# Optimization experiments

Hardware: AMD Instinct MI355X
Metric: run time of the kernel (lower is better)

The kernel has to match this reference:

```python
import jax, jax.numpy as jnp
import numpy as np

D_MODEL = 32
N_HEADS = 4
D_K = 8
D_V = 8
LN_EPS = 1e-5
MASK_FILL = -1.0e9


def _layernorm(x, eps=LN_EPS):
    # torch.nn.LayerNorm with default affine params (gamma=1, beta=0)
    mu = jnp.mean(x, axis=-1, keepdims=True)
    var = jnp.var(x, axis=-1, keepdims=True)  # biased, matches torch
    return (x - mu) * jax.lax.rsqrt(var + eps)


def setup_inputs() -> dict:
    key = jax.random.key(0)
    ks = jax.random.split(key, 12)
    B, S = 8, 2048
    w = 1.0 / np.float32(np.sqrt(D_MODEL))
    return {
        "input_Q": jax.random.normal(ks[0], (B, S, D_MODEL), dtype=jnp.float32),
        "input_K": jax.random.normal(ks[1], (B, S, D_MODEL), dtype=jnp.float32),
        "input_V": jax.random.normal(ks[2], (B, S, D_MODEL), dtype=jnp.float32),
        "attn_mask": jax.random.randint(ks[3], (B, S, S), 0, 2).astype(jnp.bool_),
        "W_Q": jax.random.normal(ks[4], (D_MODEL, D_K * N_HEADS), dtype=jnp.float32) * w,
        "b_Q": jax.random.normal(ks[5], (D_K * N_HEADS,), dtype=jnp.float32) * 0.02,
        "W_K": jax.random.normal(ks[6], (D_MODEL, D_K * N_HEADS), dtype=jnp.float32) * w,
        "b_K": jax.random.normal(ks[7], (D_K * N_HEADS,), dtype=jnp.float32) * 0.02,
        "W_V": jax.random.normal(ks[8], (D_MODEL, D_V * N_HEADS), dtype=jnp.float32) * w,
        "b_V": jax.random.normal(ks[9], (D_V * N_HEADS,), dtype=jnp.float32) * 0.02,
        "W_O": jax.random.normal(ks[10], (D_V * N_HEADS, D_MODEL), dtype=jnp.float32) * w,
        "b_O": jax.random.normal(ks[11], (D_MODEL,), dtype=jnp.float32) * 0.02,
    }


def reference(input_Q, input_K, input_V, attn_mask, W_Q, b_Q, W_K, b_K, W_V, b_V, W_O, b_O):
    B, S, _ = input_Q.shape
    residual = input_Q
    # projections -> [B, H, S, d_head]
    Q = (input_Q @ W_Q + b_Q).reshape(B, S, N_HEADS, D_K).transpose(0, 2, 1, 3)
    K = (input_K @ W_K + b_K).reshape(B, S, N_HEADS, D_K).transpose(0, 2, 1, 3)
    V = (input_V @ W_V + b_V).reshape(B, S, N_HEADS, D_V).transpose(0, 2, 1, 3)
    scale = 1.0 / jnp.sqrt(jnp.asarray(D_K, dtype=Q.dtype))
    scores = jnp.einsum("bhqd,bhkd->bhqk", Q, K) * scale  # [B,H,S,S]
    scores = jnp.where(attn_mask[:, None, :, :], jnp.asarray(MASK_FILL, scores.dtype), scores)
    attn_ratio = jax.nn.softmax(scores, axis=-1)
    ctx = jnp.einsum("bhqk,bhkd->bhqd", attn_ratio, V)  # [B,H,S,Dv]
    self_attn = ctx.transpose(0, 2, 1, 3).reshape(B, S, N_HEADS * D_V)
    attn_output = self_attn @ W_O + b_O
    return (_layernorm(attn_output + residual), self_attn)
```

## Files before the change

### kernel.cpp

```cpp
#include <hip/hip_runtime.h>
#include <math.h>

#define D_MODEL 32
#define S_LEN   2048
#define B_SZ    8
#define NTOK    (B_SZ * S_LEN)
#define LN_EPS  1e-5f
#define LOG2E   1.44269504088896340736f
#define QK_SCALE 0.35355339059327373f
#define PROJ_BLKS (NTOK / 8)

typedef __attribute__((ext_vector_type(8)))  short    short8b;
typedef __attribute__((ext_vector_type(4)))  short    short4b;
typedef __attribute__((ext_vector_type(4)))  unsigned uint4v;
typedef __attribute__((ext_vector_type(16))) float    f32x16;

__device__ __forceinline__ unsigned short f2bf(float f) {
    unsigned u = __builtin_bit_cast(unsigned, f);
    unsigned r = (u + 0x7FFFu + ((u >> 16) & 1u)) >> 16;
    return (unsigned short)r;
}
__device__ __forceinline__ float bf2f(unsigned short h) {
    return __builtin_bit_cast(float, (unsigned)h << 16);
}
__device__ __forceinline__ unsigned cvtpk_bf16(float lo, float hi) {
    unsigned r;
    asm("v_cvt_pk_bf16_f32 %0, %1, %2" : "=v"(r) : "v"(lo), "v"(hi));
    return r;
}


__global__ __launch_bounds__(256) void prep_kernel(
    const void* __restrict__ mask,
    const float* __restrict__ xQ, const float* __restrict__ xK,
    const float* __restrict__ xV,
    const float* __restrict__ WQ, const float* __restrict__ bQ,
    const float* __restrict__ WK, const float* __restrict__ bK,
    const float* __restrict__ WV, const float* __restrict__ bV,
    unsigned short* __restrict__ QHC, unsigned short* __restrict__ QLC,
    unsigned short* __restrict__ KC,  unsigned short* __restrict__ VC,
    unsigned long long* __restrict__ pack)
{
    int bid = blockIdx.x;
    int t   = threadIdx.x;

    if (bid < 3 * PROJ_BLKS) {
        int which = bid / PROJ_BLKS;
        int xb    = bid - which * PROJ_BLKS;
        const float* x; const float* W; const float* bias; float scale;
        if (which == 0)      { x = xQ; W = WQ; bias = bQ; scale = QK_SCALE * LOG2E; }
        else if (which == 1) { x = xK; W = WK; bias = bK; scale = 1.0f; }
        else                 { x = xV; W = WV; bias = bV; scale = 1.0f; }

        __shared__ float xs[8][32];
        __shared__ float Ws[32][32];
        long base = (long)xb * 256;
        xs[t >> 5][t & 31] = x[base + t];
#pragma unroll
        for (int i = 0; i < 4; ++i) {
            int f = i * 256 + t;
            Ws[f >> 5][f & 31] = W[f];
        }
        __syncthreads();
        int r = t >> 5, j = t & 31;
        float acc = bias[j];
#pragma unroll
        for (int i = 0; i < 32; ++i) acc = fmaf(xs[r][i], Ws[i][j], acc);
        acc *= scale;

        long tok = (long)xb * 8 + r;
        long b   = tok >> 11;
        long ti  = tok & (S_LEN - 1);
        int  ch  = (int)(ti >> 5), kq = (int)(ti & 31);
        int  h   = j >> 3, d = j & 7;

        if (which == 0) {
            size_t qi = ((((size_t)b * 64 + ch) * 4 + h) * 32 + kq) * 8 + d;
            unsigned short hv = f2bf(acc);
            QHC[qi] = hv;
            QLC[qi] = f2bf(acc - bf2f(hv));
        } else if (which == 1) {
            size_t ki = (((((size_t)b * 64 + ch) * 4 + h) * 2 + 0) * 32 + kq) * 8 + d;
            unsigned short hv = f2bf(acc);
            KC[ki]       = hv;
            KC[ki + 256] = f2bf(acc - bf2f(hv));
        } else {
            size_t vi = (((size_t)b * 64 + ch) * 4 + h) * 256 + (size_t)d * 32 + kq;
            VC[vi] = f2bf(acc);
        }
    } else {
        int mb   = bid - 3 * PROJ_BLKS;
        long row = (long)mb * 4 + (t >> 6);
        int lane = t & 63;

        int probe = ((const int*)mask)[lane];
        bool is32 = (__ballot((probe & ~0xFF) == 0) == ~0ULL);

        unsigned long long* prow = pack + row * (S_LEN / 64);
        if (is32) {
            const int4* mr4 = (const int4*)((const int*)mask + row * S_LEN);
#pragma unroll
            for (int g = 0; g < 8; ++g) {
                int4 v = mr4[g * 64 + lane];
                unsigned long long b0 = __ballot(v.x != 0);
                unsigned long long b1 = __ballot(v.y != 0);
                unsigned long long b2 = __ballot(v.z != 0);
                unsigned long long b3 = __ballot(v.w != 0);
                if (lane == 0) {
                    prow[g * 4 + 0] = b0; prow[g * 4 + 1] = b1;
                    prow[g * 4 + 2] = b2; prow[g * 4 + 3] = b3;
                }
            }
        } else {
            const int* mri = (const int*)((const unsigned char*)mask + row * S_LEN);
#pragma unroll
            for (int g = 0; g < 8; ++g) {
                int v = mri[g * 64 + lane];
                unsigned long long b0 = __ballot((v & 0x000000FF) != 0);
                unsigned long long b1 = __ballot((v & 0x0000FF00) != 0);
                unsigned long long b2 = __ballot((v & 0x00FF0000) != 0);
                unsigned long long b3 = __ballot((v & 0xFF000000u) != 0);
                if (lane == 0) {
                    prow[g * 4 + 0] = b0; prow[g * 4 + 1] = b1;
                    prow[g * 4 + 2] = b2; prow[g * 4 + 3] = b3;
                }
            }
        }
    }
}

template<int NSEG>
__global__ __launch_bounds__(256, 4) void attn_kernel(
    const unsigned short* __restrict__ QHC, const unsigned short* __restrict__ QLC,
    const unsigned short* __restrict__ KC,  const unsigned short* __restrict__ VC,
    const unsigned long long* __restrict__ pack,
    float* __restrict__ pl, float* __restrict__ pctx)
{
    constexpr int SEGLEN = S_LEN / NSEG;
    constexpr int NGROUP = SEGLEN / 256;
    constexpr int NPT    = SEGLEN / 64;
    const int nb    = NSEG * 64;
    int raw   = blockIdx.x;
    int total = B_SZ * nb;
    int cpx   = total >> 3;
    int cid   = (raw & 7) * cpx + (raw >> 3);
    int b     = cid / nb;
    int rem   = cid - b * nb;
    int seg   = rem >> 6;
    int qt    = rem & 63;
    int h     = threadIdx.x >> 6;
    int lane  = threadIdx.x & 63;
    int q     = lane & 31;
    int half  = lane >> 5;
    int tok0  = qt * 32;
    long tokq = (long)b * S_LEN + tok0 + q;
    int k0    = seg * SEGLEN;
    int ch0   = k0 >> 5;

    f32x16 zero16;
#pragma unroll
    for (int i = 0; i < 16; ++i) zero16[i] = 0.0f;

    const unsigned long long* prow = pack + tokq * (S_LEN / 64);

    short ovv = (q == 8) ? (short)0x3F80 : (short)0;
    short8b ovf;
#pragma unroll
    for (int i = 0; i < 8; ++i) ovf[i] = ovv;

    size_t qoff = ((((size_t)b * 64 + qt) * 4 + h) * 32 + q) * 8;
    short8b qhf = *(const short8b*)(QHC + qoff);
    short8b qlf = *(const short8b*)(QLC + qoff);
    f32x16 cpv = zero16;

    const unsigned short* Kb0 = KC + (((size_t)b * 64) * 4 + h) * 512
                                   + (size_t)half * 256 + (size_t)q * 8;
    const unsigned short* Vb0 = VC + (((size_t)b * 64) * 4 + h) * 256
                                   + (size_t)q * 32 + half * 4;

    short8b kfA = *(const short8b*)(Kb0 + (size_t)ch0 * 2048);
    short8b kfB = *(const short8b*)(Kb0 + (size_t)(ch0 + 1) * 2048);
    short8b vf1c, vf2c;
    if (q < 8) {
        const unsigned short* vr = Vb0 + (size_t)ch0 * 1024;
        short4b a0 = *(const short4b*)(vr);
        short4b a1 = *(const short4b*)(vr + 8);
        short4b a2 = *(const short4b*)(vr + 16);
        short4b a3 = *(const short4b*)(vr + 24);
        vf1c = __builtin_shufflevector(a0, a1, 0, 1, 2, 3, 4, 5, 6, 7);
        vf2c = __builtin_shufflevector(a2, a3, 0, 1, 2, 3, 4, 5, 6, 7);
    } else { vf1c = ovf; vf2c = ovf; }

#pragma unroll
    for (int g = 0; g < NGROUP; ++g) {
        unsigned long long mg[4];
        mg[0] = prow[(k0 >> 6) + g * 4 + 0];
        mg[1] = prow[(k0 >> 6) + g * 4 + 1];
        mg[2] = prow[(k0 >> 6) + g * 4 + 2];
        mg[3] = prow[(k0 >> 6) + g * 4 + 3];

#pragma unroll 1
        for (int p = 0; p < 4; ++p) {
            int pa  = g * 4 + p;
            int chA = ch0 + 2 * pa;
            int chB = chA + 1;

            short8b kfA_n = kfA, kfB_n = kfB;
            if (pa + 1 < NPT) {
                kfA_n = *(const short8b*)(Kb0 + (size_t)(chA + 2) * 2048);
                kfB_n = *(const short8b*)(Kb0 + (size_t)(chB + 2) * 2048);
            }

            unsigned shA = (unsigned)(p * 16 + half);
            unsigned nA[4], nB[4];
#pragma unroll
            for (int c = 0; c < 4; ++c) {
                nA[c] = (unsigned)(mg[c] >> shA);
                nB[c] = (unsigned)(mg[c] >> (shA + 8u));
            }

            __builtin_amdgcn_s_setprio(1);
            f32x16 accA = __builtin_amdgcn_mfma_f32_32x32x16_bf16(kfA, qhf, zero16, 0, 0, 0);
            f32x16 accB = __builtin_amdgcn_mfma_f32_32x32x16_bf16(kfB, qhf, zero16, 0, 0, 0);
            accA = __builtin_amdgcn_mfma_f32_32x32x16_bf16(kfA, qlf, accA, 0, 0, 0);
            accB = __builtin_amdgcn_mfma_f32_32x32x16_bf16(kfB, qlf, accB, 0, 0, 0);
            __builtin_amdgcn_s_setprio(0);

            short8b vf1n, vf2n;
            if (q < 8) {
                const unsigned short* vr = Vb0 + (size_t)chB * 1024;
                short4b a0 = *(const short4b*)(vr);
                short4b a1 = *(const short4b*)(vr + 8);
                short4b a2 = *(const short4b*)(vr + 16);
                short4b a3 = *(const short4b*)(vr + 24);
                vf1n = __builtin_shufflevector(a0, a1, 0, 1, 2, 3, 4, 5, 6, 7);
                vf2n = __builtin_shufflevector(a2, a3, 0, 1, 2, 3, 4, 5, 6, 7);
            } else { vf1n = ovf; vf2n = ovf; }

            {
                unsigned pr[8];
#pragma unroll
                for (int j = 0; j < 8; ++j) {
                    const int c0 = (2 * j) & 3, c1 = (2 * j + 1) & 3;
                    const int s  = 2 * (j >> 1);
                    float p0 = ((nA[c0] >> s) & 1u) ? 0.0f
                             : __builtin_amdgcn_exp2f(accA[2 * j]);
                    float p1 = ((nA[c1] >> s) & 1u) ? 0.0f
                             : __builtin_amdgcn_exp2f(accA[2 * j + 1]);
                    pr[j] = cvtpk_bf16(p0, p1);
                }
                uint4v t1, t2;
                t1.x = pr[0]; t1.y = pr[1]; t1.z = pr[2]; t1.w = pr[3];
                t2.x = pr[4]; t2.y = pr[5]; t2.z = pr[6]; t2.w = pr[7];
                short8b pfa = __builtin_bit_cast(short8b, t1);
                short8b pfb = __builtin_bit_cast(short8b, t2);

                __builtin_amdgcn_s_setprio(1);
                cpv = __builtin_amdgcn_mfma_f32_32x32x16_bf16(vf1c, pfa, cpv, 0, 0, 0);
                cpv = __builtin_amdgcn_mfma_f32_32x32x16_bf16(vf2c, pfb, cpv, 0, 0, 0);
                __builtin_amdgcn_s_setprio(0);
            }

            short8b vf1nn, vf2nn;
            if (pa + 1 < NPT && q < 8) {
                const unsigned short* vr = Vb0 + (size_t)(chA + 2) * 1024;
                short4b a0 = *(const short4b*)(vr);
                short4b a1 = *(const short4b*)(vr + 8);
                short4b a2 = *(const short4b*)(vr + 16);
                short4b a3 = *(const short4b*)(vr + 24);
                vf1nn = __builtin_shufflevector(a0, a1, 0, 1, 2, 3, 4, 5, 6, 7);
                vf2nn = __builtin_shufflevector(a2, a3, 0, 1, 2, 3, 4, 5, 6, 7);
            } else { vf1nn = ovf; vf2nn = ovf; }

            {
                unsigned pr[8];
#pragma unroll
                for (int j = 0; j < 8; ++j) {
                    const int c0 = (2 * j) & 3, c1 = (2 * j + 1) & 3;
                    const int s  = 2 * (j >> 1);
                    float p0 = ((nB[c0] >> s) & 1u) ? 0.0f
                             : __builtin_amdgcn_exp2f(accB[2 * j]);
                    float p1 = ((nB[c1] >> s) & 1u) ? 0.0f
                             : __builtin_amdgcn_exp2f(accB[2 * j + 1]);
                    pr[j] = cvtpk_bf16(p0, p1);
                }
                uint4v t1, t2;
                t1.x = pr[0]; t1.y = pr[1]; t1.z = pr[2]; t1.w = pr[3];
                t2.x = pr[4]; t2.y = pr[5]; t2.z = pr[6]; t2.w = pr[7];
                short8b pfa = __builtin_bit_cast(short8b, t1);
                short8b pfb = __builtin_bit_cast(short8b, t2);

                __builtin_amdgcn_s_setprio(1);
                cpv = __builtin_amdgcn_mfma_f32_32x32x16_bf16(vf1n, pfa, cpv, 0, 0, 0);
                cpv = __builtin_amdgcn_mfma_f32_32x32x16_bf16(vf2n, pfb, cpv, 0, 0, 0);
                __builtin_amdgcn_s_setprio(0);
            }

            kfA = kfA_n;
            kfB = kfB_n;
            vf1c = vf1nn;
            vf2c = vf2nn;
        }
    }

    float4 cv = make_float4(cpv[0], cpv[1], cpv[2], cpv[3]);
    *(float4*)(pctx + ((size_t)seg * NTOK + tokq) * 32 + h * 8 + half * 4) = cv;
    if (half == 0)
        pl[(size_t)seg * NTOK * 4 + tokq * 4 + h] = cpv[4];
}

template<int NSEG>
__global__ __launch_bounds__(256) void combine_epilogue(
    const float* __restrict__ pl, const float* __restrict__ pctx,
    const float* __restrict__ WO, const float* __restrict__ bO,
    const float* __restrict__ resid,
    float* __restrict__ sa_out, float* __restrict__ out0)
{
    __shared__ float sas[8][32];
    __shared__ float Ws[32][32];
    int t = threadIdx.x;
    long base = (long)blockIdx.x * 256;
    int r = t >> 5, j = t & 31;
    long tok = (long)blockIdx.x * 8 + r;
    int h = j >> 3;

#pragma unroll
    for (int i = 0; i < 4; ++i) {
        int f = i * 256 + t;
        Ws[f >> 5][f & 31] = WO[f];
    }

    float L = 0.f, ctx = 0.f;
#pragma unroll
    for (int s2 = 0; s2 < NSEG; ++s2) {
        L   += pl[(size_t)s2 * NTOK * 4 + tok * 4 + h];
        ctx += pctx[((size_t)s2 * NTOK + tok) * 32 + j];
    }
    float sa = ctx / L;
    sa_out[base + t] = sa;
    sas[r][j] = sa;
    __syncthreads();

    float y = bO[j] + resid[base + t];
#pragma unroll
    for (int i = 0; i < 32; ++i) y = fmaf(sas[r][i], Ws[i][j], y);

    float sum = y;
#pragma unroll
    for (int o = 16; o >= 1; o >>= 1) sum += __shfl_xor(sum, o, 32);
    float mu = sum * (1.0f / 32.0f);
    float d  = y - mu;
    float sq = d * d;
#pragma unroll
    for (int o = 16; o >= 1; o >>= 1) sq += __shfl_xor(sq, o, 32);
    float var = sq * (1.0f / 32.0f);
    out0[base + t] = d * rsqrtf(var + LN_EPS);
}

extern "C" void kernel_launch(void* const* d_in, const int* in_sizes, int n_in,
                              void* d_out, int out_size, void* d_ws, size_t ws_size,
                              hipStream_t stream)
{
    const float* inQ = (const float*)d_in[0];
    const float* inK = (const float*)d_in[1];
    const float* inV = (const float*)d_in[2];
    const void*  mask = d_in[3];
    const float* WQ = (const float*)d_in[4];
    const float* bQ = (const float*)d_in[5];
    const float* WK = (const float*)d_in[6];
    const float* bK = (const float*)d_in[7];
    const float* WV = (const float*)d_in[8];
    const float* bV = (const float*)d_in[9];
    const float* WO = (const float*)d_in[10];
    const float* bO = (const float*)d_in[11];

    float* out0 = (float*)d_out;
    float* sa   = (float*)d_out + (long)NTOK * 32;

    char* ws = (char*)d_ws;
    unsigned short* QHC = (unsigned short*)(ws + 256);
    unsigned short* QLC = QHC + (size_t)NTOK * 32;
    unsigned short* KC  = QLC + (size_t)NTOK * 32;
    unsigned short* VC  = KC  + (size_t)NTOK * 64;
    unsigned long long* pack = (unsigned long long*)(VC + (size_t)NTOK * 32);
    float* pbase = (float*)(pack + (size_t)NTOK * (S_LEN / 64));

    size_t fixed  = 256 + 5ul * NTOK * 32 * 2 + (size_t)NTOK * (S_LEN / 64) * 8;
    size_t perseg = (size_t)NTOK * 36 * 4;
    int NS = 1;
    if (fixed + 2 * perseg <= ws_size) NS = 2;

    float* pl   = pbase;
    float* pctx = pl + (long)NS * NTOK * 4;

    prep_kernel<<<3 * PROJ_BLKS + NTOK / 4, 256, 0, stream>>>(
        mask, inQ, inK, inV, WQ, bQ, WK, bK, WV, bV, QHC, QLC, KC, VC, pack);

    int cgrid = NTOK / 8;
    switch (NS) {
    case 2: {
        int agrid = B_SZ * 2 * 64;
        attn_kernel<2><<<agrid, 256, 0, stream>>>(QHC, QLC, KC, VC, pack, pl, pctx);
        combine_epilogue<2><<<cgrid, 256, 0, stream>>>(pl, pctx, WO, bO, inQ, sa, out0);
        break;
    }
    default: {
        int agrid = B_SZ * 1 * 64;
        attn_kernel<1><<<agrid, 256, 0, stream>>>(QHC, QLC, KC, VC, pack, pl, pctx);
        combine_epilogue<1><<<cgrid, 256, 0, stream>>>(pl, pctx, WO, bO, inQ, sa, out0);
        break;
    }
    }
}
```

Before: 69.65 us.

## Fuse split-K attention segments and epilogue into one 512-thread block

```diff
diff --git a/kernel.cpp b/kernel.cpp
--- a/kernel.cpp
+++ b/kernel.cpp
@@ -129,33 +129,44 @@
     }
 }
 
-template<int NSEG>
-__global__ __launch_bounds__(256, 4) void attn_kernel(
+__global__ __launch_bounds__(512, 4) void attn_fused_kernel(
     const unsigned short* __restrict__ QHC, const unsigned short* __restrict__ QLC,
     const unsigned short* __restrict__ KC,  const unsigned short* __restrict__ VC,
     const unsigned long long* __restrict__ pack,
-    float* __restrict__ pl, float* __restrict__ pctx)
+    const float* __restrict__ WO, const float* __restrict__ bO,
+    const float* __restrict__ resid,
+    float* __restrict__ sa_out, float* __restrict__ out0)
 {
-    constexpr int SEGLEN = S_LEN / NSEG;
+    constexpr int SEGLEN = 1024;
     constexpr int NGROUP = SEGLEN / 256;
     constexpr int NPT    = SEGLEN / 64;
-    const int nb    = NSEG * 64;
-    int raw   = blockIdx.x;
-    int total = B_SZ * nb;
-    int cpx   = total >> 3;
-    int cid   = (raw & 7) * cpx + (raw >> 3);
-    int b     = cid / nb;
-    int rem   = cid - b * nb;
-    int seg   = rem >> 6;
-    int qt    = rem & 63;
-    int h     = threadIdx.x >> 6;
-    int lane  = threadIdx.x & 63;
-    int q     = lane & 31;
-    int half  = lane >> 5;
-    int tok0  = qt * 32;
+    __shared__ float ctx_lds[2][32][33];
+    __shared__ float l_lds[2][32][4];
+    __shared__ float sa_lds[32][33];
+    __shared__ float Ws[32][32];
+
+    int raw  = blockIdx.x;
+    int cid  = (raw & 7) * 64 + (raw >> 3);
+    int b    = cid >> 6;
+    int qt   = cid & 63;
+    int tid  = threadIdx.x;
+    int w    = tid >> 6;
+    int h    = w & 3;
+    int seg  = w >> 2;
+    int lane = tid & 63;
+    int q    = lane & 31;
+    int half = lane >> 5;
+    int tok0 = qt * 32;
     long tokq = (long)b * S_LEN + tok0 + q;
-    int k0    = seg * SEGLEN;
-    int ch0   = k0 >> 5;
+    int k0   = seg * SEGLEN;
+    int ch0  = k0 >> 5;
+
+    Ws[(tid >> 5) + ((tid & 31) >> 5) * 0][tid & 31] = 0.0f;
+#pragma unroll
+    for (int i = 0; i < 2; ++i) {
+        int f = i * 512 + tid;
+        Ws[f >> 5][f & 31] = WO[f];
+    }
 
     f32x16 zero16;
 #pragma unroll
@@ -303,58 +314,45 @@
         }
     }
 
-    float4 cv = make_float4(cpv[0], cpv[1], cpv[2], cpv[3]);
-    *(float4*)(pctx + ((size_t)seg * NTOK + tokq) * 32 + h * 8 + half * 4) = cv;
-    if (half == 0)
-        pl[(size_t)seg * NTOK * 4 + tokq * 4 + h] = cpv[4];
-}
-
-template<int NSEG>
-__global__ __launch_bounds__(256) void combine_epilogue(
-    const float* __restrict__ pl, const float* __restrict__ pctx,
-    const float* __restrict__ WO, const float* __restrict__ bO,
-    const float* __restrict__ resid,
-    float* __restrict__ sa_out, float* __restrict__ out0)
-{
-    __shared__ float sas[8][32];
-    __shared__ float Ws[32][32];
-    int t = threadIdx.x;
-    long base = (long)blockIdx.x * 256;
-    int r = t >> 5, j = t & 31;
-    long tok = (long)blockIdx.x * 8 + r;
-    int h = j >> 3;
-
-#pragma unroll
-    for (int i = 0; i < 4; ++i) {
-        int f = i * 256 + t;
-        Ws[f >> 5][f & 31] = WO[f];
-    }
-
-    float L = 0.f, ctx = 0.f;
-#pragma unroll
-    for (int s2 = 0; s2 < NSEG; ++s2) {
-        L   += pl[(size_t)s2 * NTOK * 4 + tok * 4 + h];
-        ctx += pctx[((size_t)s2 * NTOK + tok) * 32 + j];
-    }
-    float sa = ctx / L;
-    sa_out[base + t] = sa;
-    sas[r][j] = sa;
+    ctx_lds[seg][q][h * 8 + half * 4 + 0] = cpv[0];
+    ctx_lds[seg][q][h * 8 + half * 4 + 1] = cpv[1];
+    ctx_lds[seg][q][h * 8 + half * 4 + 2] = cpv[2];
+    ctx_lds[seg][q][h * 8 + half * 4 + 3] = cpv[3];
+    if (half == 0) l_lds[seg][q][h] = cpv[4];
     __syncthreads();
 
-    float y = bO[j] + resid[base + t];
-#pragma unroll
-    for (int i = 0; i < 32; ++i) y = fmaf(sas[r][i], Ws[i][j], y);
-
-    float sum = y;
-#pragma unroll
-    for (int o = 16; o >= 1; o >>= 1) sum += __shfl_xor(sum, o, 32);
-    float mu = sum * (1.0f / 32.0f);
-    float d  = y - mu;
-    float sq = d * d;
-#pragma unroll
-    for (int o = 16; o >= 1; o >>= 1) sq += __shfl_xor(sq, o, 32);
-    float var = sq * (1.0f / 32.0f);
-    out0[base + t] = d * rsqrtf(var + LN_EPS);
+    int r = (tid >> 5) & 15;
+    int j = tid & 31;
+#pragma unroll
+    for (int pass = 0; pass < 2; ++pass) {
+        int tok = pass * 16 + r;
+        float L  = l_lds[0][tok][j >> 3] + l_lds[1][tok][j >> 3];
+        float cx = ctx_lds[0][tok][j] + ctx_lds[1][tok][j];
+        float sa = cx / L;
+        sa_lds[tok][j] = sa;
+        sa_out[((long)b * S_LEN + tok0 + tok) * 32 + j] = sa;
+    }
+    __syncthreads();
+
+#pragma unroll
+    for (int pass = 0; pass < 2; ++pass) {
+        int tok = pass * 16 + r;
+        long grow = ((long)b * S_LEN + tok0 + tok) * 32;
+        float y = bO[j] + resid[grow + j];
+#pragma unroll
+        for (int i = 0; i < 32; ++i) y = fmaf(sa_lds[tok][i], Ws[i][j], y);
+
+        float sum = y;
+#pragma unroll
+        for (int o = 16; o >= 1; o >>= 1) sum += __shfl_xor(sum, o, 32);
+        float mu = sum * (1.0f / 32.0f);
+        float d  = y - mu;
+        float sq = d * d;
+#pragma unroll
+        for (int o = 16; o >= 1; o >>= 1) sq += __shfl_xor(sq, o, 32);
+        float var = sq * (1.0f / 32.0f);
+        out0[grow + j] = d * rsqrtf(var + LN_EPS);
+    }
 }
 
 extern "C" void kernel_launch(void* const* d_in, const int* in_sizes, int n_in,
@@ -383,32 +381,10 @@
     unsigned short* KC  = QLC + (size_t)NTOK * 32;
     unsigned short* VC  = KC  + (size_t)NTOK * 64;
     unsigned long long* pack = (unsigned long long*)(VC + (size_t)NTOK * 32);
-    float* pbase = (float*)(pack + (size_t)NTOK * (S_LEN / 64));
-
-    size_t fixed  = 256 + 5ul * NTOK * 32 * 2 + (size_t)NTOK * (S_LEN / 64) * 8;
-    size_t perseg = (size_t)NTOK * 36 * 4;
-    int NS = 1;
-    if (fixed + 2 * perseg <= ws_size) NS = 2;
-
-    float* pl   = pbase;
-    float* pctx = pl + (long)NS * NTOK * 4;
 
     prep_kernel<<<3 * PROJ_BLKS + NTOK / 4, 256, 0, stream>>>(
         mask, inQ, inK, inV, WQ, bQ, WK, bK, WV, bV, QHC, QLC, KC, VC, pack);
 
-    int cgrid = NTOK / 8;
-    switch (NS) {
-    case 2: {
-        int agrid = B_SZ * 2 * 64;
-        attn_kernel<2><<<agrid, 256, 0, stream>>>(QHC, QLC, KC, VC, pack, pl, pctx);
-        combine_epilogue<2><<<cgrid, 256, 0, stream>>>(pl, pctx, WO, bO, inQ, sa, out0);
-        break;
-    }
-    default: {
-        int agrid = B_SZ * 1 * 64;
-        attn_kernel<1><<<agrid, 256, 0, stream>>>(QHC, QLC, KC, VC, pack, pl, pctx);
-        combine_epilogue<1><<<cgrid, 256, 0, stream>>>(pl, pctx, WO, bO, inQ, sa, out0);
-        break;
-    }
-    }
-}
+    attn_fused_kernel<<<B_SZ * 64, 512, 0, stream>>>(
+        QHC, QLC, KC, VC, pack, WO, bO, inQ, sa, out0);
+}
```

New measurement: 66.85 us. 4.0% less time.
